# Kernel optimization log

Hardware: AMD Instinct MI355X
Metric: run time of the kernel (lower is better)

## Reference

```python
import jax, jax.numpy as jnp
import numpy as np

B, IC, H, W = 32, 128, 112, 112
OC, K, STRIDE, PAD = 256, 3, 2, 1


def setup_inputs() -> dict:
    key = jax.random.key(0)
    kx, kw = jax.random.split(key)
    x = jax.random.normal(kx, (B, IC, H, W), dtype=jnp.float32)
    weight = jax.random.normal(kw, (OC, IC, K, K), dtype=jnp.float32) * 0.01
    bias = jnp.zeros((OC,), dtype=jnp.float32)
    return {"x": x, "weight": weight, "bias": bias}


def reference(x, weight, bias):
    # Equivalent of the nested-loop conv: standard cross-correlation,
    # stride=2, zero padding=1, NCHW / OIHW layouts.
    out = jax.lax.conv_general_dilated(
        x, weight,
        window_strides=(STRIDE, STRIDE),
        padding=[(PAD, PAD), (PAD, PAD)],
        dimension_numbers=("NCHW", "OIHW", "NCHW"),
    )
    return out + bias[None, :, None, None]
```

## Files before the change

### kernel.cpp

```cpp
#include <hip/hip_runtime.h>
#include <hip/hip_bf16.h>


#define B_    32
#define IC_   128
#define H_    112
#define W_    112
#define HW_   (H_ * W_)
#define OC_   256
#define OH_   56
#define OW_   56
#define HP    113
#define NPIX  (B_ * OH_ * OW_)
#define XT_BYTES ((size_t)B_ * HP * HP * IC_ * 2)
#define WT_BYTES ((size_t)9 * OC_ * IC_ * 2)

typedef __attribute__((ext_vector_type(8))) short bf16x8;
typedef __attribute__((ext_vector_type(4))) float f32x4;

static __device__ __forceinline__ unsigned f2bf_u(float f) {
  union { float f; unsigned u; } v; v.f = f;
  return (v.u + 0x7FFF + ((v.u >> 16) & 1)) >> 16;
}

__global__ __launch_bounds__(256) void xtrans_kernel(
    const float* __restrict__ x, unsigned short* __restrict__ xt) {
  __shared__ unsigned short lds[128 * 128];
  const int ihp = blockIdx.x;
  const int b   = blockIdx.y;
  const int tid = threadIdx.x;

  if (ihp > 0) {
    const float* xp = x + (size_t)b * IC_ * HW_ + (size_t)(ihp - 1) * W_;
#pragma unroll
    for (int it = 0; it < 16; ++it) {
      const int i  = tid + it * 256;
      const int ic = i >> 5;
      const int g  = i & 31;
      if (g < 28) {
        const float4 v = *reinterpret_cast<const float4*>(
            xp + (size_t)ic * HW_ + g * 4);
        uint2 p;
        p.x = f2bf_u(v.x) | (f2bf_u(v.y) << 16);
        p.y = f2bf_u(v.z) | (f2bf_u(v.w) << 16);
        const int gs = g ^ (((ic >> 3) & 7) << 2);
        *reinterpret_cast<uint2*>(&lds[ic * 128 + gs * 4]) = p;
      }
    }
  }
  __syncthreads();

  unsigned short* xrow = xt + ((size_t)(b * HP + ihp)) * (HP * IC_);
  const bool live = (ihp > 0);
#pragma unroll
  for (int it = 0; it < 8; ++it) {
    const int e = tid + it * 256;
    if (e >= HP * 16) break;
    const int iwp = e >> 4;
    const int icg = e & 15;
    uint4 v = {0u, 0u, 0u, 0u};
    if (live && iwp > 0) {
      const int iw  = iwp - 1;
      const int col = ((iw >> 2) ^ ((icg & 7) << 2)) * 4 + (iw & 3);
      const int r0  = icg * 8;
      unsigned u0 = lds[(r0 + 0) * 128 + col];
      unsigned u1 = lds[(r0 + 1) * 128 + col];
      unsigned u2 = lds[(r0 + 2) * 128 + col];
      unsigned u3 = lds[(r0 + 3) * 128 + col];
      unsigned u4 = lds[(r0 + 4) * 128 + col];
      unsigned u5 = lds[(r0 + 5) * 128 + col];
      unsigned u6 = lds[(r0 + 6) * 128 + col];
      unsigned u7 = lds[(r0 + 7) * 128 + col];
      v.x = u0 | (u1 << 16);
      v.y = u2 | (u3 << 16);
      v.z = u4 | (u5 << 16);
      v.w = u6 | (u7 << 16);
    }
    *reinterpret_cast<uint4*>(xrow + iwp * IC_ + icg * 8) = v;
  }
}

__global__ __launch_bounds__(256) void wtrans_kernel(
    const float* __restrict__ w, unsigned short* __restrict__ wt) {
  const int t  = blockIdx.x * 256 + threadIdx.x;
  const int oc = t >> 7;
  const int ic = t & 127;
  const float* ws = w + (size_t)t * 9;
#pragma unroll
  for (int tap = 0; tap < 9; ++tap)
    wt[((size_t)tap * OC_ + oc) * IC_ + ic] = (unsigned short)f2bf_u(ws[tap]);
}

__global__ __launch_bounds__(256) void conv_mfma_kernel(
    const unsigned short* __restrict__ xt, const unsigned short* __restrict__ wt,
    const float* __restrict__ bias, float* __restrict__ out) {
  __shared__ short Ws[128 * 32];
  __shared__ short Xs[128 * 32];

  const int tid  = threadIdx.x;
  const int wav  = tid >> 6;
  const int lane = tid & 63;

  const int mt  = blockIdx.x & 1;
  const int pt  = blockIdx.x >> 1;
  const int oc0 = mt * 128;
  const int p0  = pt * 128;

  const int l2 = lane >> 2;
  const int lc = lane & 3;
  const char* xsrc[2];
  const char* wsrc[2];
#pragma unroll
  for (int i = 0; i < 2; ++i) {
    const int pix = p0 + wav * 32 + i * 16 + l2;
    const int b   = pix / 3136;
    const int q   = pix - b * 3136;
    const int oh  = q / 56;
    const int ow  = q - oh * 56;
    const size_t e = (((size_t)b * HP + 2 * oh) * HP + 2 * ow) * IC_;
    xsrc[i] = reinterpret_cast<const char*>(xt) + e * 2 + lc * 16;
    const int ocr = oc0 + wav * 32 + i * 16 + l2;
    wsrc[i] = reinterpret_cast<const char*>(wt) + (size_t)ocr * IC_ * 2 + lc * 16;
  }
  char* xdst = reinterpret_cast<char*>(Xs) + wav * 2048;
  char* wdst = reinterpret_cast<char*>(Ws) + wav * 2048;

  const int wm  = wav >> 1;
  const int wn  = wav & 1;
  const int l15 = lane & 15;
  const int kg  = (lane >> 4) * 8;
  const short* wrow = Ws + ((wm * 64 + l15) * 32 + kg);
  const short* xrow = Xs + ((wn * 64 + l15) * 32 + kg);

  f32x4 acc[4][4] = {};

  for (int tap = 0; tap < 9; ++tap) {
    const int kh = tap / 3;
    const int kw = tap - kh * 3;
    const size_t xtap = ((size_t)(kh * HP + kw)) * IC_ * 2;
    const size_t wtap = (size_t)tap * OC_ * IC_ * 2;
#pragma unroll
    for (int icc = 0; icc < 4; ++icc) {
      const size_t xoff = xtap + (size_t)icc * 64;
      const size_t woff = wtap + (size_t)icc * 64;
      __syncthreads();
#pragma unroll
      for (int i = 0; i < 2; ++i) {
        __builtin_amdgcn_global_load_lds(
            (const __attribute__((address_space(1))) void*)(xsrc[i] + xoff),
            (__attribute__((address_space(3))) void*)(xdst + i * 1024), 16, 0, 0);
        __builtin_amdgcn_global_load_lds(
            (const __attribute__((address_space(1))) void*)(wsrc[i] + woff),
            (__attribute__((address_space(3))) void*)(wdst + i * 1024), 16, 0, 0);
      }
      __syncthreads();

      bf16x8 af[4], bfr[4];
#pragma unroll
      for (int mi = 0; mi < 4; ++mi)
        af[mi] = *reinterpret_cast<const bf16x8*>(wrow + mi * 16 * 32);
#pragma unroll
      for (int ni = 0; ni < 4; ++ni)
        bfr[ni] = *reinterpret_cast<const bf16x8*>(xrow + ni * 16 * 32);
#pragma unroll
      for (int mi = 0; mi < 4; ++mi)
#pragma unroll
        for (int ni = 0; ni < 4; ++ni)
          acc[mi][ni] = __builtin_amdgcn_mfma_f32_16x16x32_bf16(
              af[mi], bfr[ni], acc[mi][ni], 0, 0, 0);
    }
  }

#pragma unroll
  for (int mi = 0; mi < 4; ++mi) {
#pragma unroll
    for (int j = 0; j < 4; ++j) {
      const int oc = oc0 + wm * 64 + mi * 16 + (lane >> 4) * 4 + j;
      const float bv = bias[oc];
#pragma unroll
      for (int ni = 0; ni < 4; ++ni) {
        const int pix = p0 + wn * 64 + ni * 16 + l15;
        const int b   = pix / 3136;
        const int q   = pix - b * 3136;
        out[((size_t)b * OC_ + oc) * 3136 + q] = acc[mi][ni][j] + bv;
      }
    }
  }
}

__global__ __launch_bounds__(256) void conv2d_f32_kernel(
    const float* __restrict__ x, const float* __restrict__ w,
    const float* __restrict__ bias, float* __restrict__ out) {
  __shared__ float wlds[IC_ * 9][8];
  const int b   = blockIdx.z;
  const int oc0 = blockIdx.y * 8;
  const float* wsrc = w + (size_t)oc0 * (IC_ * 9);
  for (int i = threadIdx.x; i < IC_ * 9 * 8; i += 256) {
    const int j = i / (IC_ * 9);
    const int t = i - j * (IC_ * 9);
    wlds[t][j] = wsrc[(size_t)j * (IC_ * 9) + t];
  }
  __syncthreads();
  const int p  = blockIdx.x * 256 + threadIdx.x;
  const int ow = p % OW_;
  const int oh = p / OW_;
  const bool pv = (oh < OH_);
  const int ih0 = 2 * oh - 1;
  const int iw0 = 2 * ow - 1;
  const float* xb = x + (size_t)b * IC_ * HW_ + (ptrdiff_t)ih0 * W_ + iw0;
  float acc[8];
#pragma unroll
  for (int j = 0; j < 8; ++j) acc[j] = 0.f;
  for (int ic = 0; ic < IC_; ++ic) {
    const float* xc = xb + (size_t)ic * HW_;
#pragma unroll
    for (int kh = 0; kh < 3; ++kh) {
      const bool hv = pv && ((ih0 + kh) >= 0);
#pragma unroll
      for (int kw = 0; kw < 3; ++kw) {
        const bool v = hv && ((iw0 + kw) >= 0);
        const float xv = v ? xc[kh * W_ + kw] : 0.f;
        const int t = ic * 9 + kh * 3 + kw;
        const float4 w0 = *reinterpret_cast<const float4*>(&wlds[t][0]);
        const float4 w1 = *reinterpret_cast<const float4*>(&wlds[t][4]);
        acc[0] = fmaf(xv, w0.x, acc[0]); acc[1] = fmaf(xv, w0.y, acc[1]);
        acc[2] = fmaf(xv, w0.z, acc[2]); acc[3] = fmaf(xv, w0.w, acc[3]);
        acc[4] = fmaf(xv, w1.x, acc[4]); acc[5] = fmaf(xv, w1.y, acc[5]);
        acc[6] = fmaf(xv, w1.z, acc[6]); acc[7] = fmaf(xv, w1.w, acc[7]);
      }
    }
  }
  if (pv) {
#pragma unroll
    for (int j = 0; j < 8; ++j)
      out[(((size_t)(b * OC_ + oc0 + j)) * OH_ + oh) * OW_ + ow] =
          acc[j] + bias[oc0 + j];
  }
}

extern "C" void kernel_launch(void* const* d_in, const int* in_sizes, int n_in,
                              void* d_out, int out_size, void* d_ws, size_t ws_size,
                              hipStream_t stream) {
  const float* x    = (const float*)d_in[0];
  const float* w    = (const float*)d_in[1];
  const float* bias = (const float*)d_in[2];
  float* out        = (float*)d_out;

  if (ws_size >= XT_BYTES + WT_BYTES) {
    unsigned short* xt  = (unsigned short*)d_ws;
    unsigned short* wtp = (unsigned short*)((char*)d_ws + XT_BYTES);
    xtrans_kernel<<<dim3(HP, B_), 256, 0, stream>>>(x, xt);
    wtrans_kernel<<<128, 256, 0, stream>>>(w, wtp);
    conv_mfma_kernel<<<(NPIX / 128) * 2, 256, 0, stream>>>(xt, wtp, bias, out);
  } else {
    conv2d_f32_kernel<<<dim3(13, OC_ / 8, B_), 256, 0, stream>>>(x, w, bias, out);
  }
}
```

Measured before the change: 159.4 us.

## Double-buffer LDS tiles in MFMA conv and remap block IDs

Splits the LDS staging into two buffers so the async global-to-LDS loads for the next K-chunk are issued before the MFMA work on the current chunk. This halves the barriers per chunk and lets memory latency overlap with compute. It also permutes block indices in strides of 8, likely to spread neighbouring tiles across XCDs or improve cache locality. LDS use doubles to 32 KB per block, which may lower occupancy.

```diff
diff --git a/kernel.cpp b/kernel.cpp
--- a/kernel.cpp
+++ b/kernel.cpp
@@ -94,15 +94,17 @@
 __global__ __launch_bounds__(256) void conv_mfma_kernel(
     const unsigned short* __restrict__ xt, const unsigned short* __restrict__ wt,
     const float* __restrict__ bias, float* __restrict__ out) {
-  __shared__ short Ws[128 * 32];
-  __shared__ short Xs[128 * 32];
+  __shared__ short Ws[2][128 * 32];
+  __shared__ short Xs[2][128 * 32];
 
   const int tid  = threadIdx.x;
   const int wav  = tid >> 6;
   const int lane = tid & 63;
 
-  const int mt  = blockIdx.x & 1;
-  const int pt  = blockIdx.x >> 1;
+  const int bid  = blockIdx.x;
+  const int wgid = (bid & 7) * 196 + (bid >> 3);
+  const int mt  = wgid & 1;
+  const int pt  = wgid >> 1;
   const int oc0 = mt * 128;
   const int p0  = pt * 128;
 
@@ -122,53 +124,65 @@
     const int ocr = oc0 + wav * 32 + i * 16 + l2;
     wsrc[i] = reinterpret_cast<const char*>(wt) + (size_t)ocr * IC_ * 2 + lc * 16;
   }
-  char* xdst = reinterpret_cast<char*>(Xs) + wav * 2048;
-  char* wdst = reinterpret_cast<char*>(Ws) + wav * 2048;
+  char* xdst = reinterpret_cast<char*>(&Xs[0][0]) + wav * 2048;
+  char* wdst = reinterpret_cast<char*>(&Ws[0][0]) + wav * 2048;
 
   const int wm  = wav >> 1;
   const int wn  = wav & 1;
   const int l15 = lane & 15;
   const int kg  = (lane >> 4) * 8;
-  const short* wrow = Ws + ((wm * 64 + l15) * 32 + kg);
-  const short* xrow = Xs + ((wn * 64 + l15) * 32 + kg);
+  const short* wrow = &Ws[0][0] + ((wm * 64 + l15) * 32 + kg);
+  const short* xrow = &Xs[0][0] + ((wn * 64 + l15) * 32 + kg);
 
   f32x4 acc[4][4] = {};
 
-  for (int tap = 0; tap < 9; ++tap) {
+  auto stage = [&](int buf, int tap, int icc) {
     const int kh = tap / 3;
     const int kw = tap - kh * 3;
-    const size_t xtap = ((size_t)(kh * HP + kw)) * IC_ * 2;
-    const size_t wtap = (size_t)tap * OC_ * IC_ * 2;
-#pragma unroll
-    for (int icc = 0; icc < 4; ++icc) {
-      const size_t xoff = xtap + (size_t)icc * 64;
-      const size_t woff = wtap + (size_t)icc * 64;
-      __syncthreads();
-#pragma unroll
-      for (int i = 0; i < 2; ++i) {
-        __builtin_amdgcn_global_load_lds(
-            (const __attribute__((address_space(1))) void*)(xsrc[i] + xoff),
-            (__attribute__((address_space(3))) void*)(xdst + i * 1024), 16, 0, 0);
-        __builtin_amdgcn_global_load_lds(
-            (const __attribute__((address_space(1))) void*)(wsrc[i] + woff),
-            (__attribute__((address_space(3))) void*)(wdst + i * 1024), 16, 0, 0);
-      }
-      __syncthreads();
-
-      bf16x8 af[4], bfr[4];
-#pragma unroll
-      for (int mi = 0; mi < 4; ++mi)
-        af[mi] = *reinterpret_cast<const bf16x8*>(wrow + mi * 16 * 32);
+    const size_t xoff = ((size_t)(kh * HP + kw) * IC_ + icc * 32) * 2;
+    const size_t woff = ((size_t)tap * OC_ * IC_ + icc * 32) * 2;
+    char* xd = xdst + buf * (128 * 32 * 2);
+    char* wd = wdst + buf * (128 * 32 * 2);
+#pragma unroll
+    for (int i = 0; i < 2; ++i) {
+      __builtin_amdgcn_global_load_lds(
+          (const __attribute__((address_space(1))) void*)(xsrc[i] + xoff),
+          (__attribute__((address_space(3))) void*)(xd + i * 1024), 16, 0, 0);
+      __builtin_amdgcn_global_load_lds(
+          (const __attribute__((address_space(1))) void*)(wsrc[i] + woff),
+          (__attribute__((address_space(3))) void*)(wd + i * 1024), 16, 0, 0);
+    }
+  };
+
+  auto compute = [&](int buf) {
+    const short* wr = wrow + buf * (128 * 32);
+    const short* xr = xrow + buf * (128 * 32);
+    bf16x8 af[4], bfr[4];
+#pragma unroll
+    for (int mi = 0; mi < 4; ++mi)
+      af[mi] = *reinterpret_cast<const bf16x8*>(wr + mi * 16 * 32);
+#pragma unroll
+    for (int ni = 0; ni < 4; ++ni)
+      bfr[ni] = *reinterpret_cast<const bf16x8*>(xr + ni * 16 * 32);
+#pragma unroll
+    for (int mi = 0; mi < 4; ++mi)
 #pragma unroll
       for (int ni = 0; ni < 4; ++ni)
-        bfr[ni] = *reinterpret_cast<const bf16x8*>(xrow + ni * 16 * 32);
-#pragma unroll
-      for (int mi = 0; mi < 4; ++mi)
-#pragma unroll
-        for (int ni = 0; ni < 4; ++ni)
-          acc[mi][ni] = __builtin_amdgcn_mfma_f32_16x16x32_bf16(
-              af[mi], bfr[ni], acc[mi][ni], 0, 0, 0);
-    }
+        acc[mi][ni] = __builtin_amdgcn_mfma_f32_16x16x32_bf16(
+            af[mi], bfr[ni], acc[mi][ni], 0, 0, 0);
+  };
+
+  stage(0, 0, 0);
+  __syncthreads();
+
+  for (int tap = 0; tap < 9; ++tap) {
+    const bool lt = (tap == 8);
+    stage(1, tap, 1);  compute(0);  __syncthreads();
+    stage(0, tap, 2);  compute(1);  __syncthreads();
+    stage(1, tap, 3);  compute(0);  __syncthreads();
+    if (!lt) { stage(0, tap + 1, 0); }
+    compute(1);
+    if (!lt) { __syncthreads(); }
   }
 
 #pragma unroll
```

Result: no change. 157.2 us (-1.4%).
